# Kernel tuning notes

Measured on AMD Instinct MI355X. Metric: run time of the kernel, lower is better.

## Reference

```python
import jax, jax.numpy as jnp
import numpy as np

B, T, C = 8, 2048, 1024
H, D = 16, 64
DLOW = 64  # D_DECAY = D_AAA = D_MV = D_GATE = 64
EPS_LN = 1e-5


def setup_inputs() -> dict:
    key = jax.random.key(0)
    ks = jax.random.split(key, 26)
    p = lambda k, shape, s=0.02: (jax.random.normal(k, shape, jnp.float32) * s)
    u = lambda k, shape: jax.random.uniform(k, shape, jnp.float32)
    return {
        "x":   jax.random.normal(ks[0], (B, T, C), jnp.float32),
        # token-shift mix coefficients (1,1,C)
        "x_r": u(ks[1], (1, 1, C)), "x_w": u(ks[2], (1, 1, C)),
        "x_k": u(ks[3], (1, 1, C)), "x_v": u(ks[4], (1, 1, C)),
        "x_a": u(ks[5], (1, 1, C)), "x_g": u(ks[6], (1, 1, C)),
        # decay lora: w1 [C,DLOW], w2 [DLOW,H], w0 [1,1,H,1]
        "w0": p(ks[7], (1, 1, H, 1)), "w1": p(ks[8], (C, DLOW)), "w2": p(ks[9], (DLOW, H)),
        # in-context lr lora
        "a0": p(ks[10], (1, 1, H, 1)), "a1": p(ks[11], (C, DLOW)), "a2": p(ks[12], (DLOW, H)),
        # value residual lora
        "v0": p(ks[13], (1, 1, C)), "v1": p(ks[14], (C, DLOW)), "v2": p(ks[15], (DLOW, C)),
        # gate lora
        "g1": p(ks[16], (C, DLOW)), "g2": p(ks[17], (DLOW, C)),
        "k_k": 0.85 + p(ks[18], (1, 1, C)),
        "r_k": p(ks[19], (H, D)),
        # main projections, stored [in, out] so x @ W matches nn.Linear
        "Wr": p(ks[20], (C, C)), "Wk": p(ks[21], (C, C)),
        "Wv": p(ks[22], (C, C)), "Wo": p(ks[23], (C, C)),
        # GroupNorm(n_head, n_embd) affine params
        "ln_w": jnp.ones((C,), jnp.float32) + p(ks[24], (C,)),
        "ln_b": p(ks[25], (C,)),
    }


def reference(x, x_r, x_w, x_k, x_v, x_a, x_g,
              w0, w1, w2, a0, a1, a2, v0, v1, v2, g1, g2,
              k_k, r_k, Wr, Wk, Wv, Wo, ln_w, ln_b):
    Bb, Tt, Cc = x.shape
    Hh, Dd = r_k.shape
    # token shift: sx = x_t - x_{t-1} (zero-padded)
    xx = jnp.concatenate([jnp.zeros((Bb, 1, Cc), x.dtype), x[:, :-1]], axis=1)
    sx = x - xx
    xr = x + sx * x_r
    xw = x + sx * x_w
    xk = x + sx * x_k
    xv = x + sx * x_v
    xa = x + sx * x_a
    xg = x + sx * x_g

    r = (xr @ Wr).reshape(Bb, Tt, Hh, Dd)
    # decay in (0, exp(-0.5)): exp(-softplus(-(w0 + lora)) - 0.5)
    w = jnp.exp(-jax.nn.softplus(-(w0 + (jnp.tanh(xw @ w1) @ w2).reshape(Bb, Tt, Hh, 1))) - 0.5)
    k = xk @ Wk
    v = xv @ Wv
    v_res_gate = jax.nn.sigmoid(v0 + jnp.tanh(xv @ v1) @ v2)
    v = v + (v - v) * v_res_gate  # no-op, kept for faithfulness
    a = jax.nn.sigmoid(a0 + (jnp.tanh(xa @ a1) @ a2).reshape(Bb, Tt, Hh, 1))
    g = jax.nn.sigmoid(jnp.tanh(xg @ g1) @ g2)

    kk = (k * k_k).reshape(Bb, Tt, Hh, Dd)
    kk = kk / jnp.maximum(jnp.linalg.norm(kk, axis=-1, keepdims=True), 1e-12)
    vh = v.reshape(Bb, Tt, Hh, Dd)

    # WKV linear recurrence: state = state * w_t + kk_t * v_t * a_t
    kv = (kk * vh * a).astype(jnp.float32)            # [B,T,H,D]
    w_t = jnp.moveaxis(w.astype(jnp.float32), 1, 0)   # [T,B,H,1]
    kv_t = jnp.moveaxis(kv, 1, 0)                     # [T,B,H,D]

    def step(state, inputs):
        wt, kvt = inputs
        state = state * wt + kvt
        return state, state

    init = jnp.zeros((Bb, Hh, Dd), jnp.float32)
    _, states = jax.lax.scan(step, init, (w_t, kv_t))  # [T,B,H,D]
    x_wkv = jnp.moveaxis(states, 0, 1).astype(x.dtype)  # [B,T,H,D]

    x_wkv = x_wkv * r
    bonus = jnp.sum(r * kk * r_k, axis=-1, keepdims=True) * vh
    x_wkv = x_wkv + bonus  # [B,T,H,D]

    # GroupNorm(H groups over C channels), per (B*T) sample
    mean = x_wkv.mean(axis=-1, keepdims=True)
    var = x_wkv.var(axis=-1, keepdims=True)
    xn = (x_wkv - mean) * jax.lax.rsqrt(var + EPS_LN)
    xn = xn.reshape(Bb, Tt, Cc) * ln_w + ln_b

    return (xn * g) @ Wo
```

## Files before the change

kernel.cpp:

```cpp
#include <hip/hip_runtime.h>


typedef __bf16 bf16;
typedef __attribute__((ext_vector_type(8))) __bf16 bf16x8;
typedef __attribute__((ext_vector_type(4))) float f32x4;

#define TBTOK 16384
#define TSEQ  2048
#define CDIM  1024
#define HN    16
#define CHUNK 64
#define NCH   32

__device__ __forceinline__ float wredsum(float v) {
#pragma unroll
  for (int o = 32; o > 0; o >>= 1) v += __shfl_xor(v, o, 64);
  return v;
}
__device__ __forceinline__ float qredsum(float v) {
#pragma unroll
  for (int o = 8; o > 0; o >>= 1) v += __shfl_xor(v, o, 64);
  return v;
}
__device__ __forceinline__ float sigmf(float x) { return 1.f / (1.f + expf(-x)); }

__device__ __forceinline__ void gl_lds16(const bf16* g, bf16* l) {
  __builtin_amdgcn_global_load_lds(
      (const __attribute__((address_space(1))) unsigned int*)g,
      (__attribute__((address_space(3))) unsigned int*)l, 16, 0, 0);
}

__global__ __launch_bounds__(256) void prep_kern(
    const float* __restrict__ x, const float* __restrict__ mr,
    const float* __restrict__ mk, const float* __restrict__ mv,
    bf16* __restrict__ xr, bf16* __restrict__ xk, bf16* __restrict__ xv,
    bf16* __restrict__ xbf,
    const float* __restrict__ Wr, const float* __restrict__ Wk,
    const float* __restrict__ Wv, const float* __restrict__ Wo,
    const float* __restrict__ w1, const float* __restrict__ a1, const float* __restrict__ g1,
    const float* __restrict__ mw, const float* __restrict__ ma, const float* __restrict__ mg,
    const float* __restrict__ g2, const float* __restrict__ w2, const float* __restrict__ a2,
    bf16* __restrict__ WrT, bf16* __restrict__ WkT, bf16* __restrict__ WvT, bf16* __restrict__ WoT,
    bf16* __restrict__ Bcat, bf16* __restrict__ g2T,
    bf16* __restrict__ w2T, bf16* __restrict__ a2T, float* __restrict__ zpad) {
  int bid0 = blockIdx.x;
  int tid = threadIdx.x;
  if (bid0 < 8192) {
    long i8 = ((long)bid0 * 256 + tid) * 8;
    int m = (int)(i8 >> 10);
    int c = (int)(i8 & 1023);
    f32x4 x0 = *(const f32x4*)(x + i8);
    f32x4 x1 = *(const f32x4*)(x + i8 + 4);
    f32x4 p0 = {0.f, 0.f, 0.f, 0.f}, p1 = {0.f, 0.f, 0.f, 0.f};
    if ((m & (TSEQ - 1)) != 0) {
      p0 = *(const f32x4*)(x + i8 - CDIM);
      p1 = *(const f32x4*)(x + i8 - CDIM + 4);
    }
    f32x4 r0 = *(const f32x4*)(mr + c), r1 = *(const f32x4*)(mr + c + 4);
    f32x4 k0 = *(const f32x4*)(mk + c), k1 = *(const f32x4*)(mk + c + 4);
    f32x4 v0 = *(const f32x4*)(mv + c), v1 = *(const f32x4*)(mv + c + 4);
    bf16x8 or_, ok_, ov_, ox_;
#pragma unroll
    for (int j = 0; j < 4; j++) {
      float s0 = x0[j] - p0[j], s1 = x1[j] - p1[j];
      or_[j] = (bf16)(x0[j] + s0 * r0[j]); or_[4 + j] = (bf16)(x1[j] + s1 * r1[j]);
      ok_[j] = (bf16)(x0[j] + s0 * k0[j]); ok_[4 + j] = (bf16)(x1[j] + s1 * k1[j]);
      ov_[j] = (bf16)(x0[j] + s0 * v0[j]); ov_[4 + j] = (bf16)(x1[j] + s1 * v1[j]);
      ox_[j] = (bf16)x0[j];                ox_[4 + j] = (bf16)x1[j];
    }
    *(bf16x8*)(xr + i8) = or_;
    *(bf16x8*)(xk + i8) = ok_;
    *(bf16x8*)(xv + i8) = ov_;
    *(bf16x8*)(xbf + i8) = ox_;
    return;
  }
  int bid = bid0 - 8192;
  int tx = tid & 31, ty = tid >> 5;
  __shared__ bf16 tile[32][33];
  if (bid < 4096) {
    int sel = bid >> 10, t = bid & 1023;
    int k0 = (t >> 5) * 32, n0 = (t & 31) * 32;
    const float* src = sel == 0 ? Wr : (sel == 1 ? Wk : (sel == 2 ? Wv : Wo));
    bf16* dst = sel == 0 ? WrT : (sel == 1 ? WkT : (sel == 2 ? WvT : WoT));
#pragma unroll
    for (int i = 0; i < 4; i++)
      tile[ty + i * 8][tx] = (bf16)src[(long)(k0 + ty + i * 8) * 1024 + n0 + tx];
    __syncthreads();
#pragma unroll
    for (int i = 0; i < 4; i++)
      dst[(long)(n0 + ty + i * 8) * 1024 + k0 + tx] = tile[tx][ty + i * 8];
  } else if (bid < 4480) {
    int idx = bid - 4096;
    int mat = idx >> 7, rem = idx & 127;
    int half = rem >> 6, t = rem & 63;
    int k0 = (t >> 1) * 32, n0 = (t & 1) * 32;
    const float* W = mat == 0 ? w1 : (mat == 1 ? a1 : g1);
    const float* mx = mat == 0 ? mw : (mat == 1 ? ma : mg);
#pragma unroll
    for (int i = 0; i < 4; i++) {
      int k = k0 + ty + i * 8;
      float s = half == 0 ? (1.f + mx[k]) : (-mx[k]);
      tile[ty + i * 8][tx] = (bf16)(s * W[(long)k * 64 + n0 + tx]);
    }
    __syncthreads();
#pragma unroll
    for (int i = 0; i < 4; i++)
      Bcat[(long)(mat * 64 + n0 + ty + i * 8) * 2048 + half * 1024 + k0 + tx] =
          tile[tx][ty + i * 8];
  } else if (bid < 4544) {
    int t = bid - 4480;
    int k0 = (t >> 5) * 32, n0 = (t & 31) * 32;
#pragma unroll
    for (int i = 0; i < 4; i++)
      tile[ty + i * 8][tx] = (bf16)g2[(long)(k0 + ty + i * 8) * 1024 + n0 + tx];
    __syncthreads();
#pragma unroll
    for (int i = 0; i < 4; i++)
      g2T[(long)(n0 + ty + i * 8) * 64 + k0 + tx] = tile[tx][ty + i * 8];
  } else {
#pragma unroll
    for (int rep = 0; rep < 4; rep++) {
      int idx = rep * 256 + tid;
      int k = idx >> 4, h = idx & 15;
      w2T[h * 64 + k] = (bf16)w2[idx];
      a2T[h * 64 + k] = (bf16)a2[idx];
    }
    if (tid < 64) zpad[tid] = 0.f;
  }
}

template <int ACT, typename OT>
__global__ __launch_bounds__(256) void gemm128_kern(
    const bf16* __restrict__ A0, const bf16* __restrict__ A1, const bf16* __restrict__ A2,
    int apitch,
    const bf16* __restrict__ BT0, const bf16* __restrict__ BT1, const bf16* __restrict__ BT2,
    OT* __restrict__ out0, OT* __restrict__ out1, OT* __restrict__ out2,
    int opitch, int K, int nbpm) {
  int by = blockIdx.y;
  int mat = by / nbpm;
  int ncol0 = (by % nbpm) * 128;
  const bf16* Am = mat == 0 ? A0 : (mat == 1 ? A1 : A2);
  const bf16* BTm = mat == 0 ? BT0 : (mat == 1 ? BT1 : BT2);
  OT* out = mat == 0 ? out0 : (mat == 1 ? out1 : out2);
  int m0 = blockIdx.x * 128;

  __shared__ bf16 Al[128 * 64];
  __shared__ bf16 Bl[128 * 64];

  int tid = threadIdx.x;
  int w = tid >> 6, lane = tid & 63, quad = lane >> 4, lr = lane & 15;
  int wm = (w & 1) * 64, wn = (w >> 1) * 64;

  f32x4 acc[4][4] = {};

  int r0 = tid >> 3;
  int slot = tid & 7;
  int kg = (slot ^ (r0 & 7)) * 8;
  const bf16* ag = Am + (long)(m0 + r0) * apitch + kg;
  const bf16* bg = BTm + (long)(ncol0 + r0) * K + kg;
  long astep = (long)32 * apitch;
  long bstep = (long)32 * K;
  bf16* la = Al + w * 512;
  bf16* lb = Bl + w * 512;

  for (int k0 = 0; k0 < K; k0 += 64) {
#pragma unroll
    for (int s = 0; s < 4; s++) gl_lds16(ag + s * astep, la + s * 2048);
#pragma unroll
    for (int s = 0; s < 4; s++) gl_lds16(bg + s * bstep, lb + s * 2048);
    ag += 64; bg += 64;
    __syncthreads();
#pragma unroll
    for (int ko = 0; ko < 2; ko++) {
      bf16x8 af[4], bff[4];
#pragma unroll
      for (int i = 0; i < 4; i++) {
        int ra = wm + i * 16 + lr;
        af[i] = *(const bf16x8*)&Al[ra * 64 + (((ko * 4 + quad) ^ (ra & 7)) * 8)];
      }
#pragma unroll
      for (int j = 0; j < 4; j++) {
        int rb = wn + j * 16 + lr;
        bff[j] = *(const bf16x8*)&Bl[rb * 64 + (((ko * 4 + quad) ^ (rb & 7)) * 8)];
      }
#pragma unroll
      for (int i = 0; i < 4; i++)
#pragma unroll
        for (int j = 0; j < 4; j++)
          acc[i][j] = __builtin_amdgcn_mfma_f32_16x16x32_bf16(af[i], bff[j], acc[i][j], 0, 0, 0);
    }
    __syncthreads();
  }
#pragma unroll
  for (int i = 0; i < 4; i++)
#pragma unroll
    for (int j = 0; j < 4; j++)
#pragma unroll
      for (int rg = 0; rg < 4; rg++) {
        int row = m0 + wm + i * 16 + quad * 4 + rg;
        int col = ncol0 + wn + j * 16 + lr;
        float v = acc[i][j][rg];
        if (ACT == 1) v = sigmf(v);
        out[(long)row * opitch + col] = (OT)v;
      }
}

__global__ __launch_bounds__(256) void stage1_kern(
    const bf16* __restrict__ xbf, const bf16* __restrict__ Bcat,
    const float* __restrict__ zpad, const bf16* __restrict__ w2T, const bf16* __restrict__ a2T,
    const float* __restrict__ w0, const float* __restrict__ a0,
    bf16* __restrict__ t1g, float* __restrict__ w_arr, float* __restrict__ a_arr) {
  int m0 = blockIdx.x * 64;
  __shared__ bf16 Al[64 * 32];
  __shared__ bf16 Bl[192 * 32];
  __shared__ bf16 Lt1[64 * 128];

  int tid = threadIdx.x;
  int w = tid >> 6, lane = tid & 63, quad = lane >> 4, lr = lane & 15;
  int wm = w * 16;

  f32x4 acc[12] = {};

  int r0 = tid >> 2, kc0 = (tid & 3) * 8;
  int m = m0 + r0;
  const bf16* asrc = xbf + (long)m * CDIM + kc0;
  bool firstrow = (m & (TSEQ - 1)) == 0;
  const bf16* psrc = firstrow ? (const bf16*)zpad : xbf + (long)(m - 1) * CDIM + kc0;
  int pstep = firstrow ? 0 : 32;
  const bf16* bs0 = Bcat + (long)(r0)       * 2048 + kc0;
  const bf16* bs1 = Bcat + (long)(r0 + 64)  * 2048 + kc0;
  const bf16* bs2 = Bcat + (long)(r0 + 128) * 2048 + kc0;
  bf16* la = Al + w * 512;
  bf16* lb0 = Bl + w * 512;
  bf16* lb1 = Bl + 2048 + w * 512;
  bf16* lb2 = Bl + 4096 + w * 512;

#pragma unroll 1
  for (int kk = 0; kk < 64; kk++) {
    if (kk < 32) {
      gl_lds16(asrc, la);
      asrc += 32;
    } else {
      gl_lds16(psrc, la);
      psrc += pstep;
    }
    gl_lds16(bs0, lb0);
    gl_lds16(bs1, lb1);
    gl_lds16(bs2, lb2);
    bs0 += 32; bs1 += 32; bs2 += 32;
    __syncthreads();
    bf16x8 af = *(const bf16x8*)&Al[(wm + lr) * 32 + quad * 8];
#pragma unroll
    for (int nf = 0; nf < 12; nf++) {
      bf16x8 bff = *(const bf16x8*)&Bl[(nf * 16 + lr) * 32 + quad * 8];
      acc[nf] = __builtin_amdgcn_mfma_f32_16x16x32_bf16(af, bff, acc[nf], 0, 0, 0);
    }
    __syncthreads();
  }
#pragma unroll
  for (int nf = 0; nf < 12; nf++)
#pragma unroll
    for (int rg = 0; rg < 4; rg++) {
      int row = wm + quad * 4 + rg;
      float tv = tanhf(acc[nf][rg]);
      if (nf < 8) Lt1[row * 128 + nf * 16 + lr] = (bf16)tv;
      else t1g[(long)(m0 + row) * 64 + (nf - 8) * 16 + lr] = (bf16)tv;
    }
  __syncthreads();
#pragma unroll
  for (int rep = 0; rep < 4; rep++) {
    int idx = rep * 256 + tid;
    int row = idx >> 4, h = idx & 15;
    const bf16* rw = &Lt1[row * 128];
    const bf16* ra = rw + 64;
    const bf16* ww = w2T + h * 64;
    const bf16* aw = a2T + h * 64;
    float dw = 0.f, da = 0.f;
#pragma unroll
    for (int k = 0; k < 64; k++) {
      dw += (float)rw[k] * (float)ww[k];
      da += (float)ra[k] * (float)aw[k];
    }
    w_arr[h * TBTOK + m0 + row] = 0.60653066f * sigmf(w0[h] + dw);
    a_arr[h * TBTOK + m0 + row] = sigmf(a0[h] + da);
  }
}

__global__ __launch_bounds__(256) void scan1_kern(
    const bf16* __restrict__ k_buf, const bf16* __restrict__ v_buf, const bf16* __restrict__ r_buf,
    const float* __restrict__ k_k, const float* __restrict__ r_k,
    const float* __restrict__ a_arr, const float* __restrict__ w_arr,
    float* __restrict__ kv2, float* __restrict__ Parr, float* __restrict__ bonus) {
  int wid = blockIdx.x * 4 + (threadIdx.x >> 6);
  int lane = threadIdx.x & 63;
  int bh = wid >> 5, c = wid & 31;
  int b = bh >> 4, h = bh & 15;
  int mstart = b * TSEQ + c * CHUNK;
  int kc = h * 64 + lane;
  float kkc = k_k[kc], rkc = r_k[kc];
  float st = 0.f, cw = 1.f;
  long mbase = (long)mstart * CDIM + kc;
  int hm = h * TBTOK + mstart;
  long sbase = ((long)hm) * 64 + lane;
  float kf = (float)k_buf[mbase] * kkc;
  float vf = (float)v_buf[mbase];
  float rf = (float)r_buf[mbase];
  float af = a_arr[hm];
  float wt = w_arr[hm];
  for (int t = 0; t < CHUNK; t++) {
    float kf_n = 0.f, vf_n = 0.f, rf_n = 0.f, af_n = 0.f, wt_n = 0.f;
    if (t < CHUNK - 1) {
      kf_n = (float)k_buf[mbase + CDIM] * kkc;
      vf_n = (float)v_buf[mbase + CDIM];
      rf_n = (float)r_buf[mbase + CDIM];
      af_n = a_arr[hm + 1];
      wt_n = w_arr[hm + 1];
    }
    float ss = wredsum(kf * kf);
    float kkn = kf / fmaxf(sqrtf(ss), 1e-12f);
    st = st * wt + kkn * vf * af;
    kv2[sbase] = st;
    cw *= wt;
    float bs = wredsum(rf * kkn * rkc);
    if (lane == 0) {
      Parr[hm] = cw;
      bonus[(mstart + t) * HN + h] = bs;
    }
    kf = kf_n; vf = vf_n; rf = rf_n; af = af_n; wt = wt_n;
    mbase += CDIM; hm += 1; sbase += 64;
  }
}

__global__ __launch_bounds__(64) void scan2_kern(const float* __restrict__ kv2,
                                                 const float* __restrict__ Parr,
                                                 float* __restrict__ carry) {
  int bh = blockIdx.x;
  int h = bh >> 3, b = bh & 7;
  int lane = threadIdx.x;
  float S = 0.f;
  for (int c = 0; c < NCH; c++) {
    carry[(((h * 8 + b) * NCH) + c) * 64 + lane] = S;
    int mlast = b * TSEQ + c * CHUNK + (CHUNK - 1);
    float L = kv2[((long)(h * TBTOK + mlast)) * 64 + lane];
    float pw = Parr[h * TBTOK + mlast];
    S = L + pw * S;
  }
}

__global__ __launch_bounds__(256) void gate_post_kern(
    const bf16* __restrict__ t1g, const bf16* __restrict__ g2T,
    const float* __restrict__ kv2, const float* __restrict__ Parr,
    const float* __restrict__ carry, const float* __restrict__ bonus,
    bf16* __restrict__ r_buf, const bf16* __restrict__ v_buf,
    const float* __restrict__ ln_w, const float* __restrict__ ln_b) {
  int ncol0 = blockIdx.y * 128;
  int m0 = blockIdx.x * 128;

  __shared__ bf16 Al[128 * 32];
  __shared__ bf16 Bl[128 * 32];

  int tid = threadIdx.x;
  int w = tid >> 6, lane = tid & 63, quad = lane >> 4, lr = lane & 15;
  int wm = (w & 1) * 64, wn = (w >> 1) * 64;

  f32x4 acc[4][4] = {};

  int r0 = tid >> 2, kc0 = (tid & 3) * 8;
  const bf16* ag0 = t1g + (long)(m0 + r0) * 64 + kc0;
  const bf16* ag1 = ag0 + (long)64 * 64;
  const bf16* bg0 = g2T + (long)(ncol0 + r0) * 64 + kc0;
  const bf16* bg1 = bg0 + (long)64 * 64;
  bf16* la0 = Al + w * 512;
  bf16* la1 = Al + 2048 + w * 512;
  bf16* lb0 = Bl + w * 512;
  bf16* lb1 = Bl + 2048 + w * 512;

  for (int k0 = 0; k0 < 64; k0 += 32) {
    gl_lds16(ag0, la0);
    gl_lds16(ag1, la1);
    gl_lds16(bg0, lb0);
    gl_lds16(bg1, lb1);
    ag0 += 32; ag1 += 32; bg0 += 32; bg1 += 32;
    __syncthreads();
    bf16x8 af[4], bff[4];
#pragma unroll
    for (int i = 0; i < 4; i++) af[i] = *(const bf16x8*)&Al[(wm + i * 16 + lr) * 32 + quad * 8];
#pragma unroll
    for (int j = 0; j < 4; j++) bff[j] = *(const bf16x8*)&Bl[(wn + j * 16 + lr) * 32 + quad * 8];
#pragma unroll
    for (int i = 0; i < 4; i++)
#pragma unroll
      for (int j = 0; j < 4; j++)
        acc[i][j] = __builtin_amdgcn_mfma_f32_16x16x32_bf16(af[i], bff[j], acc[i][j], 0, 0, 0);
    __syncthreads();
  }

  int col0 = ncol0 + wn;
  int h = col0 >> 6;
  int b = m0 >> 11;
  int ch = ((m0 + wm) & (TSEQ - 1)) >> 6;
  float cy[4], lnwv[4], lnbv[4];
#pragma unroll
  for (int j = 0; j < 4; j++) {
    int d = j * 16 + lr;
    cy[j] = carry[((h * 8 + b) * NCH + ch) * 64 + d];
    lnwv[j] = ln_w[col0 + d];
    lnbv[j] = ln_b[col0 + d];
  }
#pragma unroll
  for (int i = 0; i < 4; i++)
#pragma unroll
    for (int rg = 0; rg < 4; rg++) {
      int row = m0 + wm + i * 16 + quad * 4 + rg;
      float pw = Parr[h * TBTOK + row];
      float bs = bonus[row * HN + h];
      long kvb = ((long)h * TBTOK + row) * 64;
      long rb = (long)row * CDIM + col0;
      float xw[4];
#pragma unroll
      for (int j = 0; j < 4; j++) {
        int d = j * 16 + lr;
        float st = kv2[kvb + d] + pw * cy[j];
        float rf = (float)r_buf[rb + d];
        float vf = (float)v_buf[rb + d];
        xw[j] = st * rf + bs * vf;
      }
      float sum = xw[0] + xw[1] + xw[2] + xw[3];
      float mn = qredsum(sum) * (1.f / 64.f);
      float vs = 0.f;
#pragma unroll
      for (int j = 0; j < 4; j++) {
        xw[j] -= mn;
        vs += xw[j] * xw[j];
      }
      float var = qredsum(vs) * (1.f / 64.f);
      float rq = rsqrtf(var + 1e-5f);
#pragma unroll
      for (int j = 0; j < 4; j++) {
        int d = j * 16 + lr;
        float y = xw[j] * rq * lnwv[j] + lnbv[j];
        float gv = sigmf(acc[i][j][rg]);
        r_buf[rb + d] = (bf16)(y * gv);
      }
    }
}

extern "C" void kernel_launch(void* const* d_in, const int* in_sizes, int n_in,
                              void* d_out, int out_size, void* d_ws, size_t ws_size,
                              hipStream_t stream) {
  const float* x    = (const float*)d_in[0];
  const float* x_r  = (const float*)d_in[1];
  const float* x_w  = (const float*)d_in[2];
  const float* x_k  = (const float*)d_in[3];
  const float* x_v  = (const float*)d_in[4];
  const float* x_a  = (const float*)d_in[5];
  const float* x_g  = (const float*)d_in[6];
  const float* w0   = (const float*)d_in[7];
  const float* w1   = (const float*)d_in[8];
  const float* w2   = (const float*)d_in[9];
  const float* a0   = (const float*)d_in[10];
  const float* a1   = (const float*)d_in[11];
  const float* a2   = (const float*)d_in[12];
  const float* g1   = (const float*)d_in[16];
  const float* g2   = (const float*)d_in[17];
  const float* k_k  = (const float*)d_in[18];
  const float* r_k  = (const float*)d_in[19];
  const float* Wr   = (const float*)d_in[20];
  const float* Wk   = (const float*)d_in[21];
  const float* Wv   = (const float*)d_in[22];
  const float* Wo   = (const float*)d_in[23];
  const float* ln_w = (const float*)d_in[24];
  const float* ln_b = (const float*)d_in[25];
  float* out = (float*)d_out;

  char* p = (char*)d_ws;
  auto carve = [&](size_t bytes) {
    void* r = (void*)p;
    p += (bytes + 255) & ~(size_t)255;
    return r;
  };
  bf16* WrT = (bf16*)carve(1024 * 1024 * 2);
  bf16* WkT = (bf16*)carve(1024 * 1024 * 2);
  bf16* WvT = (bf16*)carve(1024 * 1024 * 2);
  bf16* WoT = (bf16*)carve(1024 * 1024 * 2);
  bf16* Bcat = (bf16*)carve(192 * 2048 * 2);
  bf16* g2T  = (bf16*)carve(1024 * 64 * 2);
  bf16* w2T  = (bf16*)carve(16 * 64 * 2);
  bf16* a2T  = (bf16*)carve(16 * 64 * 2);
  float* zpad = (float*)carve(64 * 4);
  bf16* t1g   = (bf16*)carve((size_t)TBTOK * 64 * 2);
  bf16* r_buf = (bf16*)carve((size_t)TBTOK * CDIM * 2);
  bf16* k_buf = (bf16*)carve((size_t)TBTOK * CDIM * 2);
  bf16* v_buf = (bf16*)carve((size_t)TBTOK * CDIM * 2);
  float* w_arr = (float*)carve((size_t)TBTOK * HN * 4);
  float* a_arr = (float*)carve((size_t)TBTOK * HN * 4);
  float* bonus = (float*)carve((size_t)TBTOK * HN * 4);
  float* Parr  = (float*)carve((size_t)TBTOK * HN * 4);
  float* carry = (float*)carve((size_t)128 * NCH * 64 * 4);
  bf16* xr  = (bf16*)carve((size_t)TBTOK * CDIM * 2);
  bf16* xk  = (bf16*)carve((size_t)TBTOK * CDIM * 2);
  bf16* xv  = (bf16*)carve((size_t)TBTOK * CDIM * 2);
  bf16* xbf = (bf16*)carve((size_t)TBTOK * CDIM * 2);
  float* kv2 = (float*)xv;

  prep_kern<<<dim3(8192 + 4545), 256, 0, stream>>>(
      x, x_r, x_k, x_v, xr, xk, xv, xbf,
      Wr, Wk, Wv, Wo, w1, a1, g1, x_w, x_a, x_g, g2, w2, a2,
      WrT, WkT, WvT, WoT, Bcat, g2T, w2T, a2T, zpad);
  stage1_kern<<<dim3(TBTOK / 64), 256, 0, stream>>>(
      xbf, Bcat, zpad, w2T, a2T, w0, a0, t1g, w_arr, a_arr);
  gemm128_kern<0, bf16><<<dim3(TBTOK / 128, 24), 256, 0, stream>>>(
      xr, xk, xv, CDIM, WrT, WkT, WvT,
      r_buf, k_buf, v_buf, CDIM, 1024, 8);
  scan1_kern<<<dim3(128 * NCH / 4), 256, 0, stream>>>(
      k_buf, v_buf, r_buf, k_k, r_k, a_arr, w_arr, kv2, Parr, bonus);
  scan2_kern<<<dim3(128), 64, 0, stream>>>(kv2, Parr, carry);
  gate_post_kern<<<dim3(TBTOK / 128, 8), 256, 0, stream>>>(
      t1g, g2T, kv2, Parr, carry, bonus, r_buf, v_buf, ln_w, ln_b);
  gemm128_kern<0, float><<<dim3(TBTOK / 128, 8), 256, 0, stream>>>(
      r_buf, r_buf, r_buf, CDIM, WoT, WoT, WoT,
      out, out, out, CDIM, 1024, 8);
}
```

Before: 583.9 us.

## Drop carry scan, halve chunks, split stage1 and vectorize gate epilogue

Halves the WKV chunk length to 32, doubling the number of chunks. It removes the serial scan2 carry kernel: each chunk's carry now comes only from the previous chunk's local end state. This relies on the per-step decay being bounded by exp(-0.5), so contributions from older chunks are negligible. Stage1 is split across two blocks in y, one for the decay/lr LoRA and one for the gate LoRA, to add parallelism. The GEMM and gate grids are transposed for better operand locality, and the gate/GroupNorm epilogue is staged through LDS with 8-wide vector loads and stores.

```diff
diff --git a/kernel.cpp b/kernel.cpp
--- a/kernel.cpp
+++ b/kernel.cpp
@@ -9,17 +9,17 @@
 #define TSEQ  2048
 #define CDIM  1024
 #define HN    16
-#define CHUNK 64
-#define NCH   32
+#define CHUNK 32
+#define NCH   64
 
 __device__ __forceinline__ float wredsum(float v) {
 #pragma unroll
   for (int o = 32; o > 0; o >>= 1) v += __shfl_xor(v, o, 64);
   return v;
 }
-__device__ __forceinline__ float qredsum(float v) {
-#pragma unroll
-  for (int o = 8; o > 0; o >>= 1) v += __shfl_xor(v, o, 64);
+__device__ __forceinline__ float redsum8(float v) {
+#pragma unroll
+  for (int o = 4; o > 0; o >>= 1) v += __shfl_xor(v, o, 64);
   return v;
 }
 __device__ __forceinline__ float sigmf(float x) { return 1.f / (1.f + expf(-x)); }
@@ -136,13 +136,13 @@
     const bf16* __restrict__ BT0, const bf16* __restrict__ BT1, const bf16* __restrict__ BT2,
     OT* __restrict__ out0, OT* __restrict__ out1, OT* __restrict__ out2,
     int opitch, int K, int nbpm) {
-  int by = blockIdx.y;
-  int mat = by / nbpm;
-  int ncol0 = (by % nbpm) * 128;
+  int bx = blockIdx.x;
+  int mat = bx / nbpm;
+  int ncol0 = (bx % nbpm) * 128;
   const bf16* Am = mat == 0 ? A0 : (mat == 1 ? A1 : A2);
   const bf16* BTm = mat == 0 ? BT0 : (mat == 1 ? BT1 : BT2);
   OT* out = mat == 0 ? out0 : (mat == 1 ? out1 : out2);
-  int m0 = blockIdx.x * 128;
+  int m0 = blockIdx.y * 128;
 
   __shared__ bf16 Al[128 * 64];
   __shared__ bf16 Bl[128 * 64];
@@ -211,15 +211,14 @@
     const float* __restrict__ w0, const float* __restrict__ a0,
     bf16* __restrict__ t1g, float* __restrict__ w_arr, float* __restrict__ a_arr) {
   int m0 = blockIdx.x * 64;
+  int part = blockIdx.y;
   __shared__ bf16 Al[64 * 32];
-  __shared__ bf16 Bl[192 * 32];
-  __shared__ bf16 Lt1[64 * 128];
+  __shared__ bf16 Bl[128 * 32];
+  __shared__ bf16 Lt1[64 * 136];
 
   int tid = threadIdx.x;
   int w = tid >> 6, lane = tid & 63, quad = lane >> 4, lr = lane & 15;
   int wm = w * 16;
-
-  f32x4 acc[12] = {};
 
   int r0 = tid >> 2, kc0 = (tid & 3) * 8;
   int m = m0 + r0;
@@ -227,62 +226,80 @@
   bool firstrow = (m & (TSEQ - 1)) == 0;
   const bf16* psrc = firstrow ? (const bf16*)zpad : xbf + (long)(m - 1) * CDIM + kc0;
   int pstep = firstrow ? 0 : 32;
-  const bf16* bs0 = Bcat + (long)(r0)       * 2048 + kc0;
-  const bf16* bs1 = Bcat + (long)(r0 + 64)  * 2048 + kc0;
-  const bf16* bs2 = Bcat + (long)(r0 + 128) * 2048 + kc0;
+  int brow0 = part ? 128 : 0;
+  const bf16* bs0 = Bcat + (long)(brow0 + r0) * 2048 + kc0;
+  const bf16* bs1 = bs0 + (long)64 * 2048;
   bf16* la = Al + w * 512;
   bf16* lb0 = Bl + w * 512;
   bf16* lb1 = Bl + 2048 + w * 512;
-  bf16* lb2 = Bl + 4096 + w * 512;
-
+
+  if (part == 0) {
+    f32x4 acc[8] = {};
 #pragma unroll 1
-  for (int kk = 0; kk < 64; kk++) {
-    if (kk < 32) {
-      gl_lds16(asrc, la);
-      asrc += 32;
-    } else {
-      gl_lds16(psrc, la);
-      psrc += pstep;
-    }
-    gl_lds16(bs0, lb0);
-    gl_lds16(bs1, lb1);
-    gl_lds16(bs2, lb2);
-    bs0 += 32; bs1 += 32; bs2 += 32;
-    __syncthreads();
-    bf16x8 af = *(const bf16x8*)&Al[(wm + lr) * 32 + quad * 8];
-#pragma unroll
-    for (int nf = 0; nf < 12; nf++) {
-      bf16x8 bff = *(const bf16x8*)&Bl[(nf * 16 + lr) * 32 + quad * 8];
-      acc[nf] = __builtin_amdgcn_mfma_f32_16x16x32_bf16(af, bff, acc[nf], 0, 0, 0);
-    }
-    __syncthreads();
-  }
-#pragma unroll
-  for (int nf = 0; nf < 12; nf++)
-#pragma unroll
-    for (int rg = 0; rg < 4; rg++) {
-      int row = wm + quad * 4 + rg;
-      float tv = tanhf(acc[nf][rg]);
-      if (nf < 8) Lt1[row * 128 + nf * 16 + lr] = (bf16)tv;
-      else t1g[(long)(m0 + row) * 64 + (nf - 8) * 16 + lr] = (bf16)tv;
-    }
-  __syncthreads();
-#pragma unroll
-  for (int rep = 0; rep < 4; rep++) {
-    int idx = rep * 256 + tid;
-    int row = idx >> 4, h = idx & 15;
-    const bf16* rw = &Lt1[row * 128];
-    const bf16* ra = rw + 64;
-    const bf16* ww = w2T + h * 64;
-    const bf16* aw = a2T + h * 64;
-    float dw = 0.f, da = 0.f;
-#pragma unroll
-    for (int k = 0; k < 64; k++) {
-      dw += (float)rw[k] * (float)ww[k];
-      da += (float)ra[k] * (float)aw[k];
-    }
-    w_arr[h * TBTOK + m0 + row] = 0.60653066f * sigmf(w0[h] + dw);
-    a_arr[h * TBTOK + m0 + row] = sigmf(a0[h] + da);
+    for (int kk = 0; kk < 64; kk++) {
+      if (kk < 32) { gl_lds16(asrc, la); asrc += 32; }
+      else         { gl_lds16(psrc, la); psrc += pstep; }
+      gl_lds16(bs0, lb0);
+      gl_lds16(bs1, lb1);
+      bs0 += 32; bs1 += 32;
+      __syncthreads();
+      bf16x8 af = *(const bf16x8*)&Al[(wm + lr) * 32 + quad * 8];
+#pragma unroll
+      for (int nf = 0; nf < 8; nf++) {
+        bf16x8 bff = *(const bf16x8*)&Bl[(nf * 16 + lr) * 32 + quad * 8];
+        acc[nf] = __builtin_amdgcn_mfma_f32_16x16x32_bf16(af, bff, acc[nf], 0, 0, 0);
+      }
+      __syncthreads();
+    }
+#pragma unroll
+    for (int nf = 0; nf < 8; nf++)
+#pragma unroll
+      for (int rg = 0; rg < 4; rg++) {
+        int row = wm + quad * 4 + rg;
+        Lt1[row * 136 + nf * 16 + lr] = (bf16)tanhf(acc[nf][rg]);
+      }
+    __syncthreads();
+#pragma unroll
+    for (int rep = 0; rep < 4; rep++) {
+      int idx = rep * 256 + tid;
+      int row = idx >> 4, h = idx & 15;
+      const bf16* rw = &Lt1[row * 136];
+      const bf16* ra = rw + 64;
+      const bf16* ww = w2T + h * 64;
+      const bf16* aw = a2T + h * 64;
+      float dw = 0.f, da = 0.f;
+#pragma unroll
+      for (int k = 0; k < 64; k++) {
+        dw += (float)rw[k] * (float)ww[k];
+        da += (float)ra[k] * (float)aw[k];
+      }
+      w_arr[h * TBTOK + m0 + row] = 0.60653066f * sigmf(w0[h] + dw);
+      a_arr[h * TBTOK + m0 + row] = sigmf(a0[h] + da);
+    }
+  } else {
+    f32x4 acc[4] = {};
+#pragma unroll 1
+    for (int kk = 0; kk < 64; kk++) {
+      if (kk < 32) { gl_lds16(asrc, la); asrc += 32; }
+      else         { gl_lds16(psrc, la); psrc += pstep; }
+      gl_lds16(bs0, lb0);
+      bs0 += 32;
+      __syncthreads();
+      bf16x8 af = *(const bf16x8*)&Al[(wm + lr) * 32 + quad * 8];
+#pragma unroll
+      for (int nf = 0; nf < 4; nf++) {
+        bf16x8 bff = *(const bf16x8*)&Bl[(nf * 16 + lr) * 32 + quad * 8];
+        acc[nf] = __builtin_amdgcn_mfma_f32_16x16x32_bf16(af, bff, acc[nf], 0, 0, 0);
+      }
+      __syncthreads();
+    }
+#pragma unroll
+    for (int nf = 0; nf < 4; nf++)
+#pragma unroll
+      for (int rg = 0; rg < 4; rg++) {
+        int row = wm + quad * 4 + rg;
+        t1g[(long)(m0 + row) * 64 + nf * 16 + lr] = (bf16)tanhf(acc[nf][rg]);
+      }
   }
 }
 
@@ -290,10 +307,11 @@
     const bf16* __restrict__ k_buf, const bf16* __restrict__ v_buf, const bf16* __restrict__ r_buf,
     const float* __restrict__ k_k, const float* __restrict__ r_k,
     const float* __restrict__ a_arr, const float* __restrict__ w_arr,
-    float* __restrict__ kv2, float* __restrict__ Parr, float* __restrict__ bonus) {
+    float* __restrict__ kv2, float* __restrict__ Parr, float* __restrict__ bonus,
+    float* __restrict__ Lend) {
   int wid = blockIdx.x * 4 + (threadIdx.x >> 6);
   int lane = threadIdx.x & 63;
-  int bh = wid >> 5, c = wid & 31;
+  int bh = wid >> 6, c = wid & 63;
   int b = bh >> 4, h = bh & 15;
   int mstart = b * TSEQ + c * CHUNK;
   int kc = h * 64 + lane;
@@ -329,35 +347,21 @@
     kf = kf_n; vf = vf_n; rf = rf_n; af = af_n; wt = wt_n;
     mbase += CDIM; hm += 1; sbase += 64;
   }
-}
-
-__global__ __launch_bounds__(64) void scan2_kern(const float* __restrict__ kv2,
-                                                 const float* __restrict__ Parr,
-                                                 float* __restrict__ carry) {
-  int bh = blockIdx.x;
-  int h = bh >> 3, b = bh & 7;
-  int lane = threadIdx.x;
-  float S = 0.f;
-  for (int c = 0; c < NCH; c++) {
-    carry[(((h * 8 + b) * NCH) + c) * 64 + lane] = S;
-    int mlast = b * TSEQ + c * CHUNK + (CHUNK - 1);
-    float L = kv2[((long)(h * TBTOK + mlast)) * 64 + lane];
-    float pw = Parr[h * TBTOK + mlast];
-    S = L + pw * S;
-  }
+  Lend[(long)wid * 64 + lane] = st;
 }
 
 __global__ __launch_bounds__(256) void gate_post_kern(
     const bf16* __restrict__ t1g, const bf16* __restrict__ g2T,
     const float* __restrict__ kv2, const float* __restrict__ Parr,
-    const float* __restrict__ carry, const float* __restrict__ bonus,
+    const float* __restrict__ Lend, const float* __restrict__ bonus,
     bf16* __restrict__ r_buf, const bf16* __restrict__ v_buf,
     const float* __restrict__ ln_w, const float* __restrict__ ln_b) {
-  int ncol0 = blockIdx.y * 128;
-  int m0 = blockIdx.x * 128;
+  int ncol0 = blockIdx.x * 128;
+  int m0 = blockIdx.y * 128;
 
   __shared__ bf16 Al[128 * 32];
   __shared__ bf16 Bl[128 * 32];
+  __shared__ bf16 gtile[128 * 136];
 
   int tid = threadIdx.x;
   int w = tid >> 6, lane = tid & 63, quad = lane >> 4, lr = lane & 15;
@@ -394,55 +398,73 @@
         acc[i][j] = __builtin_amdgcn_mfma_f32_16x16x32_bf16(af[i], bff[j], acc[i][j], 0, 0, 0);
     __syncthreads();
   }
-
-  int col0 = ncol0 + wn;
-  int h = col0 >> 6;
-  int b = m0 >> 11;
-  int ch = ((m0 + wm) & (TSEQ - 1)) >> 6;
-  float cy[4], lnwv[4], lnbv[4];
-#pragma unroll
-  for (int j = 0; j < 4; j++) {
-    int d = j * 16 + lr;
-    cy[j] = carry[((h * 8 + b) * NCH + ch) * 64 + d];
-    lnwv[j] = ln_w[col0 + d];
-    lnbv[j] = ln_b[col0 + d];
-  }
 #pragma unroll
   for (int i = 0; i < 4; i++)
 #pragma unroll
-    for (int rg = 0; rg < 4; rg++) {
-      int row = m0 + wm + i * 16 + quad * 4 + rg;
-      float pw = Parr[h * TBTOK + row];
-      float bs = bonus[row * HN + h];
-      long kvb = ((long)h * TBTOK + row) * 64;
-      long rb = (long)row * CDIM + col0;
-      float xw[4];
-#pragma unroll
-      for (int j = 0; j < 4; j++) {
-        int d = j * 16 + lr;
-        float st = kv2[kvb + d] + pw * cy[j];
-        float rf = (float)r_buf[rb + d];
-        float vf = (float)v_buf[rb + d];
-        xw[j] = st * rf + bs * vf;
-      }
-      float sum = xw[0] + xw[1] + xw[2] + xw[3];
-      float mn = qredsum(sum) * (1.f / 64.f);
-      float vs = 0.f;
-#pragma unroll
-      for (int j = 0; j < 4; j++) {
-        xw[j] -= mn;
-        vs += xw[j] * xw[j];
-      }
-      float var = qredsum(vs) * (1.f / 64.f);
-      float rq = rsqrtf(var + 1e-5f);
-#pragma unroll
-      for (int j = 0; j < 4; j++) {
-        int d = j * 16 + lr;
-        float y = xw[j] * rq * lnwv[j] + lnbv[j];
-        float gv = sigmf(acc[i][j][rg]);
-        r_buf[rb + d] = (bf16)(y * gv);
-      }
-    }
+    for (int j = 0; j < 4; j++)
+#pragma unroll
+      for (int rg = 0; rg < 4; rg++) {
+        int row = wm + i * 16 + quad * 4 + rg;
+        int col = wn + j * 16 + lr;
+        gtile[row * 136 + col] = (bf16)sigmf(acc[i][j][rg]);
+      }
+  __syncthreads();
+
+  int c_loc = (tid & 15) * 8;
+  int col_g = ncol0 + c_loc;
+  int h = col_g >> 6;
+  int d0 = col_g & 63;
+  f32x4 lnw0 = *(const f32x4*)(ln_w + col_g);
+  f32x4 lnw1 = *(const f32x4*)(ln_w + col_g + 4);
+  f32x4 lnb0 = *(const f32x4*)(ln_b + col_g);
+  f32x4 lnb1 = *(const f32x4*)(ln_b + col_g + 4);
+#pragma unroll
+  for (int jj = 0; jj < 8; jj++) {
+    int row = jj * 16 + (tid >> 4);
+    int row_g = m0 + row;
+    int b = row_g >> 11;
+    int ch = (row_g & (TSEQ - 1)) >> 5;
+    long kvb = ((long)h * TBTOK + row_g) * 64 + d0;
+    f32x4 st0 = *(const f32x4*)(kv2 + kvb);
+    f32x4 st1 = *(const f32x4*)(kv2 + kvb + 4);
+    f32x4 cy0 = {0.f, 0.f, 0.f, 0.f}, cy1 = {0.f, 0.f, 0.f, 0.f};
+    if (ch != 0) {
+      long lb = ((long)((b * 16 + h) * NCH + ch - 1)) * 64 + d0;
+      cy0 = *(const f32x4*)(Lend + lb);
+      cy1 = *(const f32x4*)(Lend + lb + 4);
+    }
+    float pw = Parr[h * TBTOK + row_g];
+    float bs = bonus[row_g * HN + h];
+    long rb = (long)row_g * CDIM + col_g;
+    bf16x8 rf8 = *(const bf16x8*)(r_buf + rb);
+    bf16x8 vf8 = *(const bf16x8*)(v_buf + rb);
+    bf16x8 g8 = *(const bf16x8*)&gtile[row * 136 + c_loc];
+    float xw[8];
+#pragma unroll
+    for (int q = 0; q < 4; q++) {
+      xw[q]     = (st0[q] + pw * cy0[q]) * (float)rf8[q]     + bs * (float)vf8[q];
+      xw[4 + q] = (st1[q] + pw * cy1[q]) * (float)rf8[4 + q] + bs * (float)vf8[4 + q];
+    }
+    float sum = 0.f;
+#pragma unroll
+    for (int q = 0; q < 8; q++) sum += xw[q];
+    float mn = redsum8(sum) * (1.f / 64.f);
+    float vs = 0.f;
+#pragma unroll
+    for (int q = 0; q < 8; q++) {
+      xw[q] -= mn;
+      vs += xw[q] * xw[q];
+    }
+    float var = redsum8(vs) * (1.f / 64.f);
+    float rq = rsqrtf(var + 1e-5f);
+    bf16x8 o8;
+#pragma unroll
+    for (int q = 0; q < 4; q++) {
+      o8[q]     = (bf16)((xw[q] * rq * lnw0[q] + lnb0[q]) * (float)g8[q]);
+      o8[4 + q] = (bf16)((xw[4 + q] * rq * lnw1[q] + lnb1[q]) * (float)g8[4 + q]);
+    }
+    *(bf16x8*)(r_buf + rb) = o8;
+  }
 }
 
 extern "C" void kernel_launch(void* const* d_in, const int* in_sizes, int n_in,
@@ -496,7 +518,7 @@
   float* a_arr = (float*)carve((size_t)TBTOK * HN * 4);
   float* bonus = (float*)carve((size_t)TBTOK * HN * 4);
   float* Parr  = (float*)carve((size_t)TBTOK * HN * 4);
-  float* carry = (float*)carve((size_t)128 * NCH * 64 * 4);
+  float* Lend  = (float*)carve((size_t)128 * NCH * 64 * 4);
   bf16* xr  = (bf16*)carve((size_t)TBTOK * CDIM * 2);
   bf16* xk  = (bf16*)carve((size_t)TBTOK * CDIM * 2);
   bf16* xv  = (bf16*)carve((size_t)TBTOK * CDIM * 2);
@@ -507,17 +529,16 @@
       x, x_r, x_k, x_v, xr, xk, xv, xbf,
       Wr, Wk, Wv, Wo, w1, a1, g1, x_w, x_a, x_g, g2, w2, a2,
       WrT, WkT, WvT, WoT, Bcat, g2T, w2T, a2T, zpad);
-  stage1_kern<<<dim3(TBTOK / 64), 256, 0, stream>>>(
+  stage1_kern<<<dim3(TBTOK / 64, 2), 256, 0, stream>>>(
       xbf, Bcat, zpad, w2T, a2T, w0, a0, t1g, w_arr, a_arr);
-  gemm128_kern<0, bf16><<<dim3(TBTOK / 128, 24), 256, 0, stream>>>(
+  gemm128_kern<0, bf16><<<dim3(24, TBTOK / 128), 256, 0, stream>>>(
       xr, xk, xv, CDIM, WrT, WkT, WvT,
       r_buf, k_buf, v_buf, CDIM, 1024, 8);
   scan1_kern<<<dim3(128 * NCH / 4), 256, 0, stream>>>(
-      k_buf, v_buf, r_buf, k_k, r_k, a_arr, w_arr, kv2, Parr, bonus);
-  scan2_kern<<<dim3(128), 64, 0, stream>>>(kv2, Parr, carry);
-  gate_post_kern<<<dim3(TBTOK / 128, 8), 256, 0, stream>>>(
-      t1g, g2T, kv2, Parr, carry, bonus, r_buf, v_buf, ln_w, ln_b);
-  gemm128_kern<0, float><<<dim3(TBTOK / 128, 8), 256, 0, stream>>>(
+      k_buf, v_buf, r_buf, k_k, r_k, a_arr, w_arr, kv2, Parr, bonus, Lend);
+  gate_post_kern<<<dim3(8, TBTOK / 128), 256, 0, stream>>>(
+      t1g, g2T, kv2, Parr, Lend, bonus, r_buf, v_buf, ln_w, ln_b);
+  gemm128_kern<0, float><<<dim3(8, TBTOK / 128), 256, 0, stream>>>(
       r_buf, r_buf, r_buf, CDIM, WoT, WoT, WoT,
       out, out, out, CDIM, 1024, 8);
 }
```

After: 569.1 us. -2.5%, faster.
